# Kernel optimization log

Hardware: AMD Instinct MI355X
Metric: run time of the kernel (lower is better)

The kernel has to match this reference:

```python
import jax, jax.numpy as jnp
import numpy as np

B, N, F, D, H, T = 32, 1024, 32, 64, 64, 4


def setup_inputs() -> dict:
    key = jax.random.key(0)
    ks = jax.random.split(key, 12)
    def w(k, shape):
        return 0.01 * jax.random.normal(k, shape, dtype=jnp.float32)
    z = lambda *s: jnp.zeros(s, jnp.float32)
    return {
        "xv": jax.random.normal(ks[0], (B, N, F), dtype=jnp.float32),
        "option": jax.random.uniform(ks[1], (B, 1), dtype=jnp.float32),
        "adj": jax.random.normal(ks[2], (N, N), dtype=jnp.float32),
        "mu1": w(ks[3], (F, D)),
        "W2": w(ks[4], (D, D)), "b2": z(D),
        "W3": w(ks[5], (D, D)), "b3": z(D),
        "W4": w(ks[6], (D, 1)), "b4": z(D),
        "Wq1": w(ks[7], (D, D)), "bq1": z(D),
        "Wq2": w(ks[8], (D, 1)), "bq2": z(D),
        "Wreg": w(ks[9], (H, 2 * D)), "breg": z(H),
        "Wq": w(ks[10], (1, H)), "bq": z(1),
    }


def reference(xv, option, adj, mu1, W2, b2, W3, b3, W4, b4,
              Wq1, bq1, Wq2, bq2, Wreg, breg, Wq, bq):
    # binary adjacency for message passing, raw weights for the mu_4 branch
    A = (adj > 0).astype(xv.dtype)                       # [N,N]
    mu_1 = jnp.maximum(xv @ mu1, 0.0)                    # [B,N,D]
    # mu_4: Linear(1,D) over every edge weight, clamp, sum over neighbors
    # (identical value every round t>=1, so computed once)
    mu4 = jnp.maximum(adj[..., None] * W4[:, 0] + b4, 0.0).sum(axis=1)[None]  # [1,N,D]
    mu3 = mu4 @ W3.T + b3                                # [1,N,D]
    mu = mu_1                                            # t = 0
    for _ in range(1, T):                                # t = 1..T-1
        mu_pool = jnp.einsum('nm,bmd->bnd', A, mu)       # neighbor aggregation
        mu2 = mu_pool @ W2.T + b2
        mu = jnp.maximum(mu_1 + mu2 + mu3, 0.0)
    mu_mean = jnp.maximum(mu.mean(axis=1, keepdims=True) @ Wq1.T + bq1, 0.0)  # [B,1,D]
    mu_aug = jnp.concatenate([mu, mu_mean], axis=1)      # [B,N+1,D]
    q2 = option.reshape(B, 1, 1) @ Wq2.T + bq2           # [B,1,D]
    q2 = jnp.broadcast_to(q2, (B, N + 1, D))
    q_ = jnp.concatenate([mu_aug, q2], axis=-1)          # [B,N+1,2D]
    qreg = jnp.maximum(q_ @ Wreg.T + breg, 0.0)          # [B,N+1,H]
    return qreg @ Wq.T + bq                              # [B,N+1,1]
```

## Files before the change

### kernel.cpp

```cpp
#include <hip/hip_runtime.h>
#include <hip/hip_bf16.h>

#define Bc 32
#define Nc 1024
#define Fc 32
#define Dc 64
#define Hc 64

typedef __bf16 bf16;
typedef __bf16 bf16x4 __attribute__((ext_vector_type(4)));
typedef __bf16 bf16x8 __attribute__((ext_vector_type(8)));
typedef float  f32x4  __attribute__((ext_vector_type(4)));

#define AS_STRIDE 136
#define MS_STRIDE 72
#define LDS_MAIN  (2 * 64 * AS_STRIDE * 2)
#define LDS_NONF  (LDS_MAIN + 2 * 64 * MS_STRIDE * 2)
#define LDS_FIN   (LDS_NONF + 2 * 64 * MS_STRIDE * 2)

__global__ void k_prep(const float* __restrict__ adj, const float* __restrict__ W2,
                       const float* __restrict__ option, const float* __restrict__ Wq2,
                       const float* __restrict__ bq2, const float* __restrict__ Wreg,
                       const float* __restrict__ breg,
                       bf16* __restrict__ Abf, bf16* __restrict__ W2bf,
                       float* __restrict__ c2base, float* __restrict__ musum) {
    const int t = threadIdx.x;
    if (blockIdx.x < 1024) {
        const int i = blockIdx.x * 1024 + t * 4;
        const float4 a = *(const float4*)&adj[i];
        bf16x4 o;
        o[0] = (bf16)((a.x > 0.f) ? 1.f : 0.f);
        o[1] = (bf16)((a.y > 0.f) ? 1.f : 0.f);
        o[2] = (bf16)((a.z > 0.f) ? 1.f : 0.f);
        o[3] = (bf16)((a.w > 0.f) ? 1.f : 0.f);
        *(bf16x4*)&Abf[i] = o;
    } else if (blockIdx.x == 1024) {
        for (int j = t * 16; j < t * 16 + 16; ++j) W2bf[j] = (bf16)W2[j];
    } else {
        for (int i = t; i < 2048; i += 256) musum[i] = 0.f;
        for (int i = t; i < 2048; i += 256) {
            const int b = i >> 6, h = i & 63;
            const float opt = option[b];
            float a = breg[h];
#pragma unroll
            for (int j = 0; j < 64; ++j)
                a = fmaf(fmaf(opt, Wq2[j], bq2[j]), Wreg[h * 128 + 64 + j], a);
            c2base[i] = a;
        }
    }
}

__global__ void k_c3(const float* __restrict__ adj, const float* __restrict__ W4,
                     const float* __restrict__ b4, const float* __restrict__ W3,
                     const float* __restrict__ b3, const float* __restrict__ b2,
                     float* __restrict__ C3) {
    const int n = blockIdx.x, t = threadIdx.x;
    const int e = t & 63, g = t >> 6;
    __shared__ float red[256];
    __shared__ float mu4_s[64];
    const float w4e = W4[e], b4e = b4[e];
    const float* arow = adj + (size_t)n * Nc;
    float acc = 0.f;
    for (int m = g * 256; m < g * 256 + 256; ++m)
        acc += fmaxf(fmaf(arow[m], w4e, b4e), 0.f);
    red[t] = acc;
    __syncthreads();
    if (g == 0) mu4_s[e] = red[e] + red[64 + e] + red[128 + e] + red[192 + e];
    __syncthreads();
    if (t < 64) {
        const int d = t;
        float a = b3[d] + b2[d];
        for (int ee = 0; ee < 64; ++ee) a = fmaf(mu4_s[ee], W3[d * 64 + ee], a);
        C3[n * 64 + d] = a;
    }
}

__global__ void k_mu1(const float* __restrict__ xv, const float* __restrict__ w,
                      const bf16* __restrict__ W2bf,
                      float* __restrict__ mu_1, bf16* __restrict__ Xt) {
    const int nb = blockIdx.x, b = blockIdx.y, t = threadIdx.x;
    const int n0 = nb * 64;
    __shared__ float w_s[Fc * Dc];
    __shared__ float x_s[64 * 33];
    __shared__ bf16  muS[64 * MS_STRIDE];
    __shared__ bf16  W2s[64 * MS_STRIDE];
    for (int i = t; i < Fc * Dc; i += 256) w_s[i] = w[i];
    for (int i = t; i < 64 * Fc; i += 256) {
        int r = i >> 5, f = i & 31;
        x_s[r * 33 + f] = xv[((size_t)b * Nc + n0 + r) * Fc + f];
    }
#pragma unroll
    for (int i = 0; i < 2; ++i) {
        int g = i * 256 + t, row = g >> 3, c = g & 7;
        *(bf16x8*)&W2s[row * MS_STRIDE + c * 8] = *(const bf16x8*)&W2bf[row * 64 + c * 8];
    }
    __syncthreads();
    const int d = t & 63, rg = t >> 6;
    for (int ri = 0; ri < 16; ++ri) {
        int r = rg * 16 + ri;
        float acc = 0.f;
#pragma unroll
        for (int f = 0; f < Fc; ++f) acc = fmaf(x_s[r * 33 + f], w_s[f * Dc + d], acc);
        acc = fmaxf(acc, 0.f);
        mu_1[((size_t)b * Nc + n0 + r) * Dc + d] = acc;
        muS[r * MS_STRIDE + d] = (bf16)acc;
    }
    __syncthreads();
    const int l = t & 63, wv = t >> 6, lm = l & 15, q = l >> 4;
    f32x4 xacc[4];
#pragma unroll
    for (int ct = 0; ct < 4; ++ct)
#pragma unroll
        for (int r = 0; r < 4; ++r) xacc[ct][r] = 0.f;
#pragma unroll
    for (int s = 0; s < 2; ++s) {
        bf16x8 a = *(const bf16x8*)&muS[(wv * 16 + lm) * MS_STRIDE + s * 32 + q * 8];
#pragma unroll
        for (int ct = 0; ct < 4; ++ct) {
            bf16x8 bv = *(const bf16x8*)&W2s[(ct * 16 + lm) * MS_STRIDE + s * 32 + q * 8];
            xacc[ct] = __builtin_amdgcn_mfma_f32_16x16x32_bf16(a, bv, xacc[ct], 0, 0, 0);
        }
    }
#pragma unroll
    for (int ct = 0; ct < 4; ++ct) {
        const int dd = ct * 16 + lm;
        bf16x4 p;
#pragma unroll
        for (int r = 0; r < 4; ++r) p[r] = (bf16)xacc[ct][r];
        *(bf16x4*)&Xt[(size_t)b * 65536 + (size_t)dd * 1024 + n0 + wv * 16 + q * 4] = p;
    }
}

template <bool FINAL>
__global__ void k_round(const bf16* __restrict__ Abf, const bf16* __restrict__ Xt_in,
                        const float* __restrict__ mu_1, const float* __restrict__ C3,
                        const bf16* __restrict__ W2bf, bf16* __restrict__ Xt_out,
                        const float* __restrict__ Wreg, const float* __restrict__ c2base,
                        const float* __restrict__ Wq, const float* __restrict__ bq,
                        float* __restrict__ musum, float* __restrict__ out) {
    const int nb = blockIdx.x, b = blockIdx.y, t = threadIdx.x;
    const int n0 = nb * 64;
    const int l = t & 63, wv = t >> 6, lm = l & 15, q = l >> 4;
    extern __shared__ char smem[];
    bf16* As   = (bf16*)smem;
    bf16* Xs   = As + 64 * AS_STRIDE;
    bf16* muHi = Xs + 64 * AS_STRIDE;
    bf16* WHi  = muHi + 64 * MS_STRIDE;
    bf16* muLo = WHi + 64 * MS_STRIDE;
    bf16* WLo  = muLo + 64 * MS_STRIDE;

    if (!FINAL) {
#pragma unroll
        for (int i = 0; i < 2; ++i) {
            int g = i * 256 + t, row = g >> 3, c = g & 7;
            *(bf16x8*)&WHi[row * MS_STRIDE + c * 8] = *(const bf16x8*)&W2bf[row * 64 + c * 8];
        }
    } else {
#pragma unroll
        for (int i = 0; i < 4; ++i) {
            int g = i * 1024 + t * 4;
            int h = g >> 6, d = g & 63;
            const float4 w4 = *(const float4*)&Wreg[h * 128 + d];
            bf16x4 ohi, olo;
            ohi[0] = (bf16)w4.x; olo[0] = (bf16)(w4.x - (float)ohi[0]);
            ohi[1] = (bf16)w4.y; olo[1] = (bf16)(w4.y - (float)ohi[1]);
            ohi[2] = (bf16)w4.z; olo[2] = (bf16)(w4.z - (float)ohi[2]);
            ohi[3] = (bf16)w4.w; olo[3] = (bf16)(w4.w - (float)ohi[3]);
            *(bf16x4*)&WHi[h * MS_STRIDE + d] = ohi;
            *(bf16x4*)&WLo[h * MS_STRIDE + d] = olo;
        }
    }

    f32x4 acc[4];
#pragma unroll
    for (int ct = 0; ct < 4; ++ct)
#pragma unroll
        for (int r = 0; r < 4; ++r) acc[ct][r] = 0.f;

    const bf16* Arow = Abf + (size_t)n0 * 1024;
    const bf16* Xrow = Xt_in + (size_t)b * 65536;
    for (int kc = 0; kc < 1024; kc += 128) {
#pragma unroll
        for (int i = 0; i < 4; ++i) {
            int g = i * 256 + t, row = g >> 4, c = g & 15;
            *(bf16x8*)&As[row * AS_STRIDE + c * 8] =
                *(const bf16x8*)&Arow[(size_t)row * 1024 + kc + c * 8];
            *(bf16x8*)&Xs[row * AS_STRIDE + c * 8] =
                *(const bf16x8*)&Xrow[(size_t)row * 1024 + kc + c * 8];
        }
        __syncthreads();
#pragma unroll
        for (int s = 0; s < 4; ++s) {
            bf16x8 a = *(const bf16x8*)&As[(wv * 16 + lm) * AS_STRIDE + s * 32 + q * 8];
#pragma unroll
            for (int ct = 0; ct < 4; ++ct) {
                bf16x8 bv = *(const bf16x8*)&Xs[(ct * 16 + lm) * AS_STRIDE + s * 32 + q * 8];
                acc[ct] = __builtin_amdgcn_mfma_f32_16x16x32_bf16(a, bv, acc[ct], 0, 0, 0);
            }
        }
        __syncthreads();
    }

    float vals[4][4];
#pragma unroll
    for (int ct = 0; ct < 4; ++ct) {
        const int col = ct * 16 + lm;
#pragma unroll
        for (int r = 0; r < 4; ++r) {
            const int n = n0 + wv * 16 + q * 4 + r;
            float v = mu_1[((size_t)b * Nc + n) * Dc + col] + acc[ct][r] + C3[n * 64 + col];
            vals[ct][r] = fmaxf(v, 0.f);
        }
    }

#pragma unroll
    for (int ct = 0; ct < 4; ++ct) {
        const int col = ct * 16 + lm;
#pragma unroll
        for (int r = 0; r < 4; ++r) {
            const int row = wv * 16 + q * 4 + r;
            const float v = vals[ct][r];
            const bf16 hi = (bf16)v;
            muHi[row * MS_STRIDE + col] = hi;
            if (FINAL) muLo[row * MS_STRIDE + col] = (bf16)(v - (float)hi);
        }
    }

    if (FINAL) {
#pragma unroll
        for (int ct = 0; ct < 4; ++ct) {
            float s = vals[ct][0] + vals[ct][1] + vals[ct][2] + vals[ct][3];
            s += __shfl_xor(s, 16);
            s += __shfl_xor(s, 32);
            if (q == 0) atomicAdd(&musum[b * 64 + ct * 16 + lm], s);
        }
    }

    __syncthreads();
    f32x4 xacc[4];
#pragma unroll
    for (int ct = 0; ct < 4; ++ct)
#pragma unroll
        for (int r = 0; r < 4; ++r) xacc[ct][r] = 0.f;

    if (!FINAL) {
#pragma unroll
        for (int s = 0; s < 2; ++s) {
            bf16x8 a = *(const bf16x8*)&muHi[(wv * 16 + lm) * MS_STRIDE + s * 32 + q * 8];
#pragma unroll
            for (int ct = 0; ct < 4; ++ct) {
                bf16x8 bv = *(const bf16x8*)&WHi[(ct * 16 + lm) * MS_STRIDE + s * 32 + q * 8];
                xacc[ct] = __builtin_amdgcn_mfma_f32_16x16x32_bf16(a, bv, xacc[ct], 0, 0, 0);
            }
        }
#pragma unroll
        for (int ct = 0; ct < 4; ++ct) {
            const int dd = ct * 16 + lm;
            bf16x4 p;
#pragma unroll
            for (int r = 0; r < 4; ++r) p[r] = (bf16)xacc[ct][r];
            *(bf16x4*)&Xt_out[(size_t)b * 65536 + (size_t)dd * 1024 + n0 + wv * 16 + q * 4] = p;
        }
    } else {
#pragma unroll
        for (int s = 0; s < 2; ++s) {
            const int aoff = (wv * 16 + lm) * MS_STRIDE + s * 32 + q * 8;
            bf16x8 aHi = *(const bf16x8*)&muHi[aoff];
            bf16x8 aLo = *(const bf16x8*)&muLo[aoff];
#pragma unroll
            for (int ct = 0; ct < 4; ++ct) {
                const int boff = (ct * 16 + lm) * MS_STRIDE + s * 32 + q * 8;
                bf16x8 bHi = *(const bf16x8*)&WHi[boff];
                bf16x8 bLo = *(const bf16x8*)&WLo[boff];
                xacc[ct] = __builtin_amdgcn_mfma_f32_16x16x32_bf16(aHi, bHi, xacc[ct], 0, 0, 0);
                xacc[ct] = __builtin_amdgcn_mfma_f32_16x16x32_bf16(aLo, bHi, xacc[ct], 0, 0, 0);
                xacc[ct] = __builtin_amdgcn_mfma_f32_16x16x32_bf16(aHi, bLo, xacc[ct], 0, 0, 0);
            }
        }
        const float bq0 = bq[0];
        float rowsum[4] = {0.f, 0.f, 0.f, 0.f};
#pragma unroll
        for (int ct = 0; ct < 4; ++ct) {
            const int h = ct * 16 + lm;
            const float c2 = c2base[b * 64 + h];
            const float wqh = Wq[h];
#pragma unroll
            for (int r = 0; r < 4; ++r)
                rowsum[r] += fmaxf(xacc[ct][r] + c2, 0.f) * wqh;
        }
#pragma unroll
        for (int r = 0; r < 4; ++r) {
            float v = rowsum[r];
            v += __shfl_xor(v, 1);
            v += __shfl_xor(v, 2);
            v += __shfl_xor(v, 4);
            v += __shfl_xor(v, 8);
            if (lm == 0) {
                const int n = n0 + wv * 16 + q * 4 + r;
                out[(size_t)b * (Nc + 1) + n] = v + bq0;
            }
        }
    }
}

__global__ void k_tail(const float* __restrict__ musum, const float* __restrict__ Wq1,
                       const float* __restrict__ bq1, const float* __restrict__ Wreg,
                       const float* __restrict__ c2base, const float* __restrict__ Wq,
                       const float* __restrict__ bq, float* __restrict__ out) {
    const int b = blockIdx.x, l = threadIdx.x;
    __shared__ float mean_s[64];
    __shared__ float mp[64];
    mean_s[l] = musum[b * 64 + l] * (1.f / Nc);
    __syncthreads();
    float a = bq1[l];
#pragma unroll
    for (int e = 0; e < 64; ++e) a = fmaf(mean_s[e], Wq1[l * 64 + e], a);
    mp[l] = fmaxf(a, 0.f);
    __syncthreads();
    float h = c2base[b * 64 + l];
#pragma unroll
    for (int d = 0; d < 64; ++d) h = fmaf(mp[d], Wreg[l * 128 + d], h);
    float v = fmaxf(h, 0.f) * Wq[l];
#pragma unroll
    for (int off = 32; off; off >>= 1) v += __shfl_down(v, off);
    if (l == 0) out[(size_t)b * (Nc + 1) + Nc] = v + bq[0];
}

extern "C" void kernel_launch(void* const* d_in, const int* in_sizes, int n_in,
                              void* d_out, int out_size, void* d_ws, size_t ws_size,
                              hipStream_t stream) {
    const float* xv     = (const float*)d_in[0];
    const float* option = (const float*)d_in[1];
    const float* adj    = (const float*)d_in[2];
    const float* mu1w   = (const float*)d_in[3];
    const float* W2     = (const float*)d_in[4];
    const float* b2     = (const float*)d_in[5];
    const float* W3     = (const float*)d_in[6];
    const float* b3     = (const float*)d_in[7];
    const float* W4     = (const float*)d_in[8];
    const float* b4     = (const float*)d_in[9];
    const float* Wq1    = (const float*)d_in[10];
    const float* bq1    = (const float*)d_in[11];
    const float* Wq2    = (const float*)d_in[12];
    const float* bq2    = (const float*)d_in[13];
    const float* Wreg   = (const float*)d_in[14];
    const float* breg   = (const float*)d_in[15];
    const float* Wq     = (const float*)d_in[16];
    const float* bq     = (const float*)d_in[17];
    float* out = (float*)d_out;

    float* ws = (float*)d_ws;
    const size_t MU = (size_t)Bc * Nc * Dc;
    float* mu_1     = ws;
    float* C3       = ws + MU;
    float* c2base   = C3 + 65536;
    float* musum    = c2base + 2048;
    bf16*  Abf      = (bf16*)(musum + 2048);
    bf16*  W2bf     = Abf + (size_t)Nc * Nc;
    bf16*  Xt0      = W2bf + 4096;
    bf16*  Xt1      = Xt0 + MU;

    k_prep<<<1026, 256, 0, stream>>>(adj, W2, option, Wq2, bq2, Wreg, breg,
                                     Abf, W2bf, c2base, musum);
    k_c3<<<Nc, 256, 0, stream>>>(adj, W4, b4, W3, b3, b2, C3);
    k_mu1<<<dim3(Nc / 64, Bc), 256, 0, stream>>>(xv, mu1w, W2bf, mu_1, Xt0);
    k_round<false><<<dim3(Nc / 64, Bc), 256, LDS_NONF, stream>>>(
        Abf, Xt0, mu_1, C3, W2bf, Xt1,
        nullptr, nullptr, nullptr, nullptr, nullptr, nullptr);
    k_round<false><<<dim3(Nc / 64, Bc), 256, LDS_NONF, stream>>>(
        Abf, Xt1, mu_1, C3, W2bf, Xt0,
        nullptr, nullptr, nullptr, nullptr, nullptr, nullptr);
    k_round<true><<<dim3(Nc / 64, Bc), 256, LDS_FIN, stream>>>(
        Abf, Xt0, mu_1, C3, nullptr, nullptr,
        Wreg, c2base, Wq, bq, musum, out);
    k_tail<<<Bc, 64, 0, stream>>>(musum, Wq1, bq1, Wreg, c2base, Wq, bq, out);
}
```

Baseline: 179.0 us.

## Register-prefetch next K-tile in k_round, swap grid order, add launch bounds

The aggregation loop in k_round now loads the next 128-wide K chunk of A and X into registers while MFMAs run on the current LDS tile, so global latency overlaps with compute. The grid is transposed so consecutive blocks share the same A row tile across batches, aiming for better L2 reuse of the adjacency matrix. Launch bounds of 256 threads with 2 blocks per SM cap register use. The prefetch buffers add register pressure, and a sync was moved to protect LDS reuse in the epilogue.

```diff
diff --git a/kernel.cpp b/kernel.cpp
--- a/kernel.cpp
+++ b/kernel.cpp
@@ -132,13 +132,14 @@
 }
 
 template <bool FINAL>
-__global__ void k_round(const bf16* __restrict__ Abf, const bf16* __restrict__ Xt_in,
-                        const float* __restrict__ mu_1, const float* __restrict__ C3,
-                        const bf16* __restrict__ W2bf, bf16* __restrict__ Xt_out,
-                        const float* __restrict__ Wreg, const float* __restrict__ c2base,
-                        const float* __restrict__ Wq, const float* __restrict__ bq,
-                        float* __restrict__ musum, float* __restrict__ out) {
-    const int nb = blockIdx.x, b = blockIdx.y, t = threadIdx.x;
+__global__ __launch_bounds__(256, 2)
+void k_round(const bf16* __restrict__ Abf, const bf16* __restrict__ Xt_in,
+             const float* __restrict__ mu_1, const float* __restrict__ C3,
+             const bf16* __restrict__ W2bf, bf16* __restrict__ Xt_out,
+             const float* __restrict__ Wreg, const float* __restrict__ c2base,
+             const float* __restrict__ Wq, const float* __restrict__ bq,
+             float* __restrict__ musum, float* __restrict__ out) {
+    const int b = blockIdx.x, nb = blockIdx.y, t = threadIdx.x;
     const int n0 = nb * 64;
     const int l = t & 63, wv = t >> 6, lm = l & 15, q = l >> 4;
     extern __shared__ char smem[];
@@ -179,16 +180,32 @@
 
     const bf16* Arow = Abf + (size_t)n0 * 1024;
     const bf16* Xrow = Xt_in + (size_t)b * 65536;
+
+    bf16x8 pa[4], px[4];
+#pragma unroll
+    for (int i = 0; i < 4; ++i) {
+        int g = i * 256 + t, row = g >> 4, c = g & 15;
+        pa[i] = *(const bf16x8*)&Arow[(size_t)row * 1024 + c * 8];
+        px[i] = *(const bf16x8*)&Xrow[(size_t)row * 1024 + c * 8];
+    }
+
     for (int kc = 0; kc < 1024; kc += 128) {
+        __syncthreads();
 #pragma unroll
         for (int i = 0; i < 4; ++i) {
             int g = i * 256 + t, row = g >> 4, c = g & 15;
-            *(bf16x8*)&As[row * AS_STRIDE + c * 8] =
-                *(const bf16x8*)&Arow[(size_t)row * 1024 + kc + c * 8];
-            *(bf16x8*)&Xs[row * AS_STRIDE + c * 8] =
-                *(const bf16x8*)&Xrow[(size_t)row * 1024 + kc + c * 8];
+            *(bf16x8*)&As[row * AS_STRIDE + c * 8] = pa[i];
+            *(bf16x8*)&Xs[row * AS_STRIDE + c * 8] = px[i];
         }
         __syncthreads();
+        if (kc + 128 < 1024) {
+#pragma unroll
+            for (int i = 0; i < 4; ++i) {
+                int g = i * 256 + t, row = g >> 4, c = g & 15;
+                pa[i] = *(const bf16x8*)&Arow[(size_t)row * 1024 + kc + 128 + c * 8];
+                px[i] = *(const bf16x8*)&Xrow[(size_t)row * 1024 + kc + 128 + c * 8];
+            }
+        }
 #pragma unroll
         for (int s = 0; s < 4; ++s) {
             bf16x8 a = *(const bf16x8*)&As[(wv * 16 + lm) * AS_STRIDE + s * 32 + q * 8];
@@ -198,7 +215,6 @@
                 acc[ct] = __builtin_amdgcn_mfma_f32_16x16x32_bf16(a, bv, acc[ct], 0, 0, 0);
             }
         }
-        __syncthreads();
     }
 
     float vals[4][4];
@@ -213,6 +229,7 @@
         }
     }
 
+    __syncthreads();
 #pragma unroll
     for (int ct = 0; ct < 4; ++ct) {
         const int col = ct * 16 + lm;
@@ -364,13 +381,13 @@
                                      Abf, W2bf, c2base, musum);
     k_c3<<<Nc, 256, 0, stream>>>(adj, W4, b4, W3, b3, b2, C3);
     k_mu1<<<dim3(Nc / 64, Bc), 256, 0, stream>>>(xv, mu1w, W2bf, mu_1, Xt0);
-    k_round<false><<<dim3(Nc / 64, Bc), 256, LDS_NONF, stream>>>(
+    k_round<false><<<dim3(Bc, Nc / 64), 256, LDS_NONF, stream>>>(
         Abf, Xt0, mu_1, C3, W2bf, Xt1,
         nullptr, nullptr, nullptr, nullptr, nullptr, nullptr);
-    k_round<false><<<dim3(Nc / 64, Bc), 256, LDS_NONF, stream>>>(
+    k_round<false><<<dim3(Bc, Nc / 64), 256, LDS_NONF, stream>>>(
         Abf, Xt1, mu_1, C3, W2bf, Xt0,
         nullptr, nullptr, nullptr, nullptr, nullptr, nullptr);
-    k_round<true><<<dim3(Nc / 64, Bc), 256, LDS_FIN, stream>>>(
+    k_round<true><<<dim3(Bc, Nc / 64), 256, LDS_FIN, stream>>>(
         Abf, Xt0, mu_1, C3, nullptr, nullptr,
         Wreg, c2base, Wq, bq, musum, out);
     k_tail<<<Bc, 64, 0, stream>>>(musum, Wq1, bq1, Wreg, c2base, Wq, bq, out);
```

Result: faster. 175.1 us (-2.2%).
